# Kernel optimization log

Hardware: AMD Instinct MI355X
Metric: run time of the kernel (lower is better)

Reference implementation:

```python
import jax, jax.numpy as jnp
import numpy as np

N, D, L = 8192, 512, 32


def setup_inputs() -> dict:
    key = jax.random.key(0)
    ks = jax.random.split(key, 14)
    def lin(k, fan_out, fan_in):
        s = 1.0 / np.sqrt(fan_in)
        kw, kb = jax.random.split(k)
        W = jax.random.uniform(kw, (fan_out, fan_in), jnp.float32, -s, s)
        b = jax.random.uniform(kb, (fan_out,), jnp.float32, -s, s)
        return W, b
    xs = jax.random.normal(ks[0], (N, D), jnp.float32)
    W1, b1 = lin(ks[1], 64, D)
    W2, b2 = lin(ks[2], 32, 64)
    W3, b3 = lin(ks[3], L, 32)
    D1, d1 = lin(ks[4], 32, L)
    D2, d2 = lin(ks[5], 64, 32)
    D3, d3 = lin(ks[6], D, 64)
    return {"xs": xs, "W1": W1, "b1": b1, "W2": W2, "b2": b2, "W3": W3, "b3": b3,
            "D1": D1, "d1": d1, "D2": D2, "d2": d2, "D3": D3, "d3": d3}


def reference(xs, W1, b1, W2, b2, W3, b3, D1, d1, D2, d2, D3, d3):
    # Nearest-neighbor (excluding self). Squared distances via Gram trick;
    # argmin over squared dists == argmin over norms, and the original's
    # +1e6*eye diagonal penalty == masking the diagonal with +inf.
    sq = jnp.sum(xs * xs, axis=-1)                     # [N]
    d2m = sq[:, None] + sq[None, :] - 2.0 * (xs @ xs.T)  # [N, N]
    d2m = d2m + jnp.where(jnp.eye(xs.shape[0], dtype=bool), jnp.inf, 0.0)
    closest = jnp.argmin(d2m, axis=1)                  # [N]
    x0s = xs[closest]                                  # [N, D]

    def encoder(x):  # batched tiny MLP, linear in jvp
        h = jax.nn.relu(x @ W1.T + b1)
        h = jax.nn.relu(h @ W2.T + b2)
        return h @ W3.T + b3

    # First-order Taylor expansion around the nearest neighbor:
    # z = f(x0) + Jf(x0) @ (x - x0)
    z0, dz = jax.jvp(encoder, (x0s,), (xs - x0s,))
    zs = z0 + dz                                       # [N, L]

    h = jax.nn.relu(zs @ D1.T + d1)
    h = jax.nn.relu(h @ D2.T + d2)
    x_hats = h @ D3.T + d3                             # [N, D]
    return (x_hats, zs)
```

## Files before the change

### kernel.cpp

```cpp
#include <hip/hip_runtime.h>
#include <hip/hip_bf16.h>

#define NROWS 8192
#define DIM 512
#define NSLOT 194
#define KMASK 0xFFFFE000u
#define QSCALE 21.0f
#define QD2 (-2.0f / (QSCALE * QSCALE))

typedef __attribute__((ext_vector_type(8))) short bf16x8;
typedef __attribute__((ext_vector_type(4))) float f32x4;
typedef __attribute__((ext_vector_type(4))) int i32x4;
typedef __attribute__((ext_vector_type(8))) unsigned short u16x8;

__device__ __forceinline__ float bf2f(unsigned short u) {
    return __uint_as_float(((unsigned int)u) << 16);
}
__device__ __forceinline__ unsigned short f2bf(float f) {
    unsigned int b = __float_as_uint(f);
    return (unsigned short)((b + 0x7FFFu + ((b >> 16) & 1u)) >> 16);
}
__device__ __forceinline__ unsigned char f2i8(float x) {
    float s = x * QSCALE;
    s = fminf(fmaxf(s, -127.f), 127.f);
    const int q = __float2int_rn(s);
    return (unsigned char)(q & 0xFF);
}
__device__ __forceinline__ unsigned int fkey(float f) {
    unsigned int b = __float_as_uint(f);
    return (b & 0x80000000u) ? ~b : (b | 0x80000000u);
}
__device__ __forceinline__ float unfkey(unsigned int u) {
    unsigned int b = (u & 0x80000000u) ? (u ^ 0x80000000u) : ~u;
    return __uint_as_float(b);
}
__device__ __forceinline__ unsigned int minu(unsigned int a, unsigned int b) {
    return a < b ? a : b;
}
__device__ __forceinline__ unsigned int maxu(unsigned int a, unsigned int b) {
    return a > b ? a : b;
}
__device__ __forceinline__ unsigned long long min64(unsigned long long a,
                                                    unsigned long long b) {
    return a < b ? a : b;
}
__device__ __forceinline__ float bcastf(float v, int k) {
    return __uint_as_float((unsigned int)__builtin_amdgcn_readlane(__float_as_uint(v), k));
}

__device__ __forceinline__ void split3(const float* v, u16x8& h8, u16x8& m8, u16x8& l8) {
#pragma unroll
    for (int j = 0; j < 8; ++j) {
        const float x = v[j];
        const unsigned short h = f2bf(x);
        const float r1 = x - bf2f(h);
        const unsigned short m = f2bf(r1);
        const float r2 = r1 - bf2f(m);
        h8[j] = h; m8[j] = m; l8[j] = f2bf(r2);
    }
}
__device__ __forceinline__ void split2(const float* v, u16x8& h8, u16x8& l8) {
#pragma unroll
    for (int j = 0; j < 8; ++j) {
        const float x = v[j];
        const unsigned short h = f2bf(x);
        h8[j] = h; l8[j] = f2bf(x - bf2f(h));
    }
}

__global__ __launch_bounds__(256) void k_prep_p(const float* __restrict__ xs,
                                                unsigned char* __restrict__ x8,
                                                float* __restrict__ sq,
                                                const float* __restrict__ W1,
                                                float* __restrict__ P) {
    __shared__ __align__(16) unsigned short lAh[64 * 32], lAm[64 * 32], lAl[64 * 32];
    __shared__ __align__(16) unsigned short lWh[64 * 32], lWm[64 * 32], lWl[64 * 32];
    const int tid = threadIdx.x;
    if (blockIdx.x >= 128) {
        const int wave = tid >> 6, lane = tid & 63;
        const int row = (blockIdx.x - 128) * 4 + wave;
        const float4* xr = (const float4*)(xs + (size_t)row * DIM);
        const float4 a = xr[2 * lane], b = xr[2 * lane + 1];
        float v[8] = {a.x, a.y, a.z, a.w, b.x, b.y, b.z, b.w};
        unsigned long long pk8 = 0ull;
        float s = 0.f;
#pragma unroll
        for (int i = 0; i < 8; ++i) {
            pk8 |= ((unsigned long long)f2i8(v[i])) << (8 * i);
            s = fmaf(v[i], v[i], s);
        }
        *(unsigned long long*)(x8 + (size_t)row * DIM + lane * 8) = pk8;
#pragma unroll
        for (int d = 32; d; d >>= 1) s += __shfl_xor(s, d);
        if (lane == 0) sq[row] = s;
        return;
    }
    const int wave = tid >> 6, lane = tid & 63, quad = lane >> 4, ln = lane & 15;
    const int i0 = blockIdx.x * 64;
    const int row = tid >> 2, c = tid & 3;
    const int wofs = row * 32 + ((c + (row >> 1)) & 3) * 8;

    f32x4 acc[4];
#pragma unroll
    for (int ns = 0; ns < 4; ++ns) acc[ns] = (f32x4){0.f, 0.f, 0.f, 0.f};

    const int ar = wave * 16 + ln;
    const int aofs = ar * 32 + ((quad + (ar >> 1)) & 3) * 8;
    int bofs[4];
#pragma unroll
    for (int ns = 0; ns < 4; ++ns) {
        const int br = ns * 16 + ln;
        bofs[ns] = br * 32 + ((quad + (br >> 1)) & 3) * 8;
    }

    for (int kt = 0; kt < 16; ++kt) {
        __syncthreads();
        {
            const float* src = xs + (size_t)(i0 + row) * DIM + kt * 32 + c * 8;
            const float4 f0 = *(const float4*)src, f1 = *(const float4*)(src + 4);
            float v[8] = {f0.x, f0.y, f0.z, f0.w, f1.x, f1.y, f1.z, f1.w};
            u16x8 h8, m8, l8;
            split3(v, h8, m8, l8);
            *(u16x8*)(lAh + wofs) = h8;
            *(u16x8*)(lAm + wofs) = m8;
            *(u16x8*)(lAl + wofs) = l8;
        }
        {
            const float* src = W1 + (size_t)row * DIM + kt * 32 + c * 8;
            const float4 f0 = *(const float4*)src, f1 = *(const float4*)(src + 4);
            float v[8] = {f0.x, f0.y, f0.z, f0.w, f1.x, f1.y, f1.z, f1.w};
            u16x8 h8, m8, l8;
            split3(v, h8, m8, l8);
            *(u16x8*)(lWh + wofs) = h8;
            *(u16x8*)(lWm + wofs) = m8;
            *(u16x8*)(lWl + wofs) = l8;
        }
        __syncthreads();
        const bf16x8 ah = *(const bf16x8*)(lAh + aofs);
        const bf16x8 am = *(const bf16x8*)(lAm + aofs);
        const bf16x8 al = *(const bf16x8*)(lAl + aofs);
#pragma unroll
        for (int ns = 0; ns < 4; ++ns) {
            const bf16x8 bh = *(const bf16x8*)(lWh + bofs[ns]);
            const bf16x8 bm = *(const bf16x8*)(lWm + bofs[ns]);
            const bf16x8 bl = *(const bf16x8*)(lWl + bofs[ns]);
            acc[ns] = __builtin_amdgcn_mfma_f32_16x16x32_bf16(ah, bh, acc[ns], 0, 0, 0);
            acc[ns] = __builtin_amdgcn_mfma_f32_16x16x32_bf16(ah, bm, acc[ns], 0, 0, 0);
            acc[ns] = __builtin_amdgcn_mfma_f32_16x16x32_bf16(am, bh, acc[ns], 0, 0, 0);
            acc[ns] = __builtin_amdgcn_mfma_f32_16x16x32_bf16(am, bm, acc[ns], 0, 0, 0);
            acc[ns] = __builtin_amdgcn_mfma_f32_16x16x32_bf16(ah, bl, acc[ns], 0, 0, 0);
            acc[ns] = __builtin_amdgcn_mfma_f32_16x16x32_bf16(al, bh, acc[ns], 0, 0, 0);
        }
    }
#pragma unroll
    for (int ns = 0; ns < 4; ++ns)
#pragma unroll
        for (int v = 0; v < 4; ++v)
            P[(size_t)(i0 + wave * 16 + quad * 4 + v) * 64 + ns * 16 + ln] = acc[ns][v];
}

__global__ __launch_bounds__(512, 4) void k_nn(const unsigned char* __restrict__ x8,
                                               const float* __restrict__ sq,
                                               unsigned int* __restrict__ rowtab) {
    __shared__ __align__(16) unsigned char lsm[32768];
    unsigned char* lA = lsm;
    unsigned char* lB = lsm + 16384;
    const int tid = threadIdx.x;
    const int wave = tid >> 6, lane = tid & 63, quad = lane >> 4, ln = lane & 15;
    const int b = blockIdx.x;
    const int xcd = b & 7, w = b >> 3;
    const int s = w >> 3, bil = w & 7;
    const int bi = xcd * 8 + bil;
    const int bj = (bi + s) & 63;
    const int i0 = bi * 128, j0 = bj * 128;
    const int m_off = (wave >> 1) * 32, n_off = (wave & 1) * 64;

    const int rl = lane >> 2;
    const int sp = ((lane & 3) - ((rl >> 1) & 3)) & 3;
    const unsigned char* gpA = x8 + (size_t)(i0 + wave * 16 + rl) * DIM + sp * 16;
    const unsigned char* gpB = x8 + (size_t)(j0 + wave * 16 + rl) * DIM + sp * 16;
    unsigned char* dstA = lA + wave * 1024;
    unsigned char* dstB = lB + wave * 1024;

    int aoff[2], boff[4];
#pragma unroll
    for (int ms = 0; ms < 2; ++ms) {
        const int r = m_off + ms * 16 + ln;
        aoff[ms] = r * 64 + ((quad + ((r >> 1) & 3)) & 3) * 16;
    }
#pragma unroll
    for (int ns = 0; ns < 4; ++ns) {
        const int r = n_off + ns * 16 + ln;
        boff[ns] = r * 64 + ((quad + ((r >> 1) & 3)) & 3) * 16;
    }

    i32x4 acc[2][4];
#pragma unroll
    for (int a = 0; a < 2; ++a)
#pragma unroll
        for (int c = 0; c < 4; ++c) acc[a][c] = (i32x4){0, 0, 0, 0};

    __builtin_amdgcn_global_load_lds(
        (const __attribute__((address_space(1))) void*)gpA,
        (__attribute__((address_space(3))) void*)dstA, 16, 0, 0);
    __builtin_amdgcn_global_load_lds(
        (const __attribute__((address_space(1))) void*)gpB,
        (__attribute__((address_space(3))) void*)dstB, 16, 0, 0);

#pragma unroll
    for (int kt = 0; kt < 8; ++kt) {
        __syncthreads();
        if (kt < 7) {
            const int nxt = ((kt + 1) & 1) * 8192;
            __builtin_amdgcn_global_load_lds(
                (const __attribute__((address_space(1))) void*)(gpA + (kt + 1) * 64),
                (__attribute__((address_space(3))) void*)(dstA + nxt), 16, 0, 0);
            __builtin_amdgcn_global_load_lds(
                (const __attribute__((address_space(1))) void*)(gpB + (kt + 1) * 64),
                (__attribute__((address_space(3))) void*)(dstB + nxt), 16, 0, 0);
        }
        const int cur = (kt & 1) * 8192;
        i32x4 av[2], bv[4];
#pragma unroll
        for (int ms = 0; ms < 2; ++ms)
            av[ms] = *(const i32x4*)(lA + cur + aoff[ms]);
#pragma unroll
        for (int ns = 0; ns < 4; ++ns)
            bv[ns] = *(const i32x4*)(lB + cur + boff[ns]);
#pragma unroll
        for (int ms = 0; ms < 2; ++ms)
#pragma unroll
            for (int ns = 0; ns < 4; ++ns)
                acc[ms][ns] = __builtin_amdgcn_mfma_i32_16x16x64_i8(
                    av[ms], bv[ns], acc[ms][ns], 0, 0, 0);
    }
    __syncthreads();

    const bool diag = (s == 0);
    float sqj[4];
#pragma unroll
    for (int ns = 0; ns < 4; ++ns) sqj[ns] = sq[j0 + n_off + ns * 16 + ln];
    float sqi[2][4];
#pragma unroll
    for (int ms = 0; ms < 2; ++ms)
#pragma unroll
        for (int v = 0; v < 4; ++v)
            sqi[ms][v] = sq[i0 + m_off + ms * 16 + quad * 4 + v];

    unsigned long long* rowbuf = (unsigned long long*)(void*)lsm + (size_t)wave * 512;

    unsigned int c1[4], c2[4];
#pragma unroll
    for (int ns = 0; ns < 4; ++ns) { c1[ns] = 0xFFFFFFFFu; c2[ns] = 0xFFFFFFFFu; }

#pragma unroll
    for (int ms = 0; ms < 2; ++ms)
#pragma unroll
        for (int v = 0; v < 4; ++v) {
            const int gi = i0 + m_off + ms * 16 + quad * 4 + v;
            const float si = sqi[ms][v];
            unsigned int rp[4];
#pragma unroll
            for (int ns = 0; ns < 4; ++ns) {
                const int gj = j0 + n_off + ns * 16 + ln;
                float d2 = fmaf((float)acc[ms][ns][v], QD2, si + sqj[ns]);
                if (diag && gj == gi) d2 = __builtin_inff();
                const unsigned int ub = (__float_as_uint(d2) | 0x80000000u) & KMASK;
                rp[ns] = ub | (unsigned int)gj;
                const unsigned int cp = ub | (unsigned int)gi;
                c2[ns] = minu(c2[ns], maxu(c1[ns], cp));
                c1[ns] = minu(c1[ns], cp);
            }
            const unsigned int lo1 = minu(rp[0], rp[1]), hi1 = maxu(rp[0], rp[1]);
            const unsigned int lo2 = minu(rp[2], rp[3]), hi2 = maxu(rp[2], rp[3]);
            const unsigned int p1 = minu(lo1, lo2);
            const unsigned int p2 = minu(maxu(lo1, lo2), minu(hi1, hi2));
            const int rloc = ms * 16 + quad * 4 + v;
            rowbuf[rloc * 16 + ln] = (((unsigned long long)p1) << 32) | p2;
        }
    asm volatile("s_waitcnt lgkmcnt(0)" ::: "memory");

    {
        const int rr = lane & 31, hf = lane >> 5;
        unsigned int p1 = 0xFFFFFFFFu, p2 = 0xFFFFFFFFu;
#pragma unroll
        for (int k = 0; k < 8; ++k) {
            const int pos = hf * 8 + (k ^ (rr & 7));
            const unsigned long long pw = rowbuf[rr * 16 + pos];
            const unsigned int a1 = (unsigned int)(pw >> 32), a2 = (unsigned int)pw;
            p2 = minu(minu(p2, a2), maxu(p1, a1));
            p1 = minu(p1, a1);
        }
        const unsigned long long mine = (((unsigned long long)p1) << 32) | p2;
        const unsigned long long oth = __shfl_xor(mine, 32);
        {
            const unsigned int a1 = (unsigned int)(oth >> 32), a2 = (unsigned int)oth;
            p2 = minu(minu(p2, a2), maxu(p1, a1));
            p1 = minu(p1, a1);
        }
        if (lane < 32) {
            const int gi = i0 + m_off + rr;
            const size_t base = ((size_t)gi * NSLOT + (s * 2 + (wave & 1))) * 2;
            rowtab[base] = p1;
            rowtab[base + 1] = p2;
        }
    }

    if (s > 0) {
#pragma unroll
        for (int ns = 0; ns < 4; ++ns) {
            unsigned int q1 = c1[ns], q2 = c2[ns];
#pragma unroll
            for (int d = 16; d <= 32; d <<= 1) {
                const unsigned long long pr = (((unsigned long long)q1) << 32) | q2;
                const unsigned long long o = __shfl_xor(pr, d);
                const unsigned int a1 = (unsigned int)(o >> 32), a2 = (unsigned int)o;
                q2 = minu(minu(q2, a2), maxu(q1, a1));
                q1 = minu(q1, a1);
            }
            if (lane < 16) {
                const int gj = j0 + n_off + ns * 16 + ln;
                const size_t base =
                    ((size_t)gj * NSLOT + (66 + (s - 1) * 4 + (wave >> 1))) * 2;
                rowtab[base] = q1;
                rowtab[base + 1] = q2;
            }
        }
    }
}

__global__ __launch_bounds__(512, 6) void k_refine_mid(
    const unsigned int* __restrict__ rowtab, const float* __restrict__ xs,
    const float* __restrict__ sq, const float* __restrict__ P,
    const float* __restrict__ b1, const float* __restrict__ W2,
    const float* __restrict__ b2, const float* __restrict__ W3,
    const float* __restrict__ b3, const float* __restrict__ D1,
    const float* __restrict__ d1, const float* __restrict__ D2,
    const float* __restrict__ d2, float* __restrict__ out_zs,
    float* __restrict__ G2) {
    __shared__ float W2T[64 * 33], W3T[32 * 33], D1T[32 * 33], D2T[32 * 65];
    __shared__ float b2f[32], b3f[32], d1f[32], d2f[64];
    __shared__ unsigned int clist[4][64];
    __shared__ int ccnt[4];
    __shared__ unsigned int rowbest[4];
    __shared__ unsigned int nnr_s[4];
    __shared__ float pbuf[4][64 * 8];
    const int tid = threadIdx.x;
    const int wave = tid >> 6, lane = tid & 63;
    const int r = wave & 3, half = wave >> 2;
    const int row = blockIdx.x * 4 + r;
    for (int t = tid; t < 2048; t += 512) { int o = t >> 6, k = t & 63; W2T[k * 33 + o] = W2[t]; }
    for (int t = tid; t < 1024; t += 512) { int o = t >> 5, k = t & 31; W3T[k * 33 + o] = W3[t]; }
    for (int t = tid; t < 1024; t += 512) { int o = t >> 5, k = t & 31; D1T[k * 33 + o] = D1[t]; }
    for (int t = tid; t < 2048; t += 512) { int o = t >> 5, k = t & 31; D2T[k * 65 + o] = D2[t]; }
    if (tid < 32) b2f[tid] = b2[tid];
    else if (tid < 64) b3f[tid - 32] = b3[tid - 32];
    else if (tid < 96) d1f[tid - 64] = d1[tid - 64];
    else if (tid < 160) d2f[tid - 96] = d2[tid - 96];
    if (tid < 4) { ccnt[tid] = 0; rowbest[tid] = 0xFFFFFFFFu; }
    __syncthreads();

    unsigned int vals[4];
    int nv = 0;
    unsigned int best = 0xFFFFFFFFu;
    for (int i = half * 64 + lane; i < NSLOT * 2; i += 128) {
        const unsigned int v = rowtab[(size_t)row * NSLOT * 2 + i];
        vals[nv++] = v;
        best = minu(best, v);
    }
#pragma unroll
    for (int d = 1; d < 64; d <<= 1) best = minu(best, __shfl_xor(best, d));
    if (lane == 0) atomicMin(&rowbest[r], best);
    __syncthreads();
    best = rowbest[r];

    const float dmin = unfkey(best & KMASK);
    const unsigned int tkey = fkey(dmin + 5.0f);
    for (int k = 0; k < nv; ++k)
        if ((vals[k] & KMASK) < tkey) {
            const int p = atomicAdd(&ccnt[r], 1);
            if (p < 64) clist[r][p] = vals[k] & 8191u;
        }
    __syncthreads();
    int cnt = ccnt[r];
    cnt = cnt > 64 ? 64 : cnt;

    const float4* xi = (const float4*)(xs + (size_t)row * DIM);
    const float4 x0 = xi[2 * lane], x1 = xi[2 * lane + 1];
    const float sqi = sq[row];
    const int g8 = lane >> 3;
    float4 cy0 = {0.f, 0.f, 0.f, 0.f}, cy1 = {0.f, 0.f, 0.f, 0.f};
    if (half < cnt) {
        const float4* xj = (const float4*)(xs + (size_t)clist[r][half] * DIM);
        cy0 = xj[2 * lane];
        cy1 = xj[2 * lane + 1];
    }
    for (int c = half; c < cnt; c += 2) {
        float4 ny0 = {0.f, 0.f, 0.f, 0.f}, ny1 = {0.f, 0.f, 0.f, 0.f};
        const int cn = c + 2;
        if (cn < cnt) {
            const float4* xj = (const float4*)(xs + (size_t)clist[r][cn] * DIM);
            ny0 = xj[2 * lane];
            ny1 = xj[2 * lane + 1];
        }
        float dot = 0.f;
        dot = fmaf(x0.x, cy0.x, dot); dot = fmaf(x0.y, cy0.y, dot);
        dot = fmaf(x0.z, cy0.z, dot); dot = fmaf(x0.w, cy0.w, dot);
        dot = fmaf(x1.x, cy1.x, dot); dot = fmaf(x1.y, cy1.y, dot);
        dot = fmaf(x1.z, cy1.z, dot); dot = fmaf(x1.w, cy1.w, dot);
        dot += __shfl_xor(dot, 1);
        dot += __shfl_xor(dot, 2);
        dot += __shfl_xor(dot, 4);
        if ((lane & 7) == 0) pbuf[r][c * 8 + g8] = dot;
        cy0 = ny0;
        cy1 = ny1;
    }
    __syncthreads();

    if (half == 0) {
        unsigned long long key = ~0ull;
        if (lane < cnt) {
            const unsigned int j = clist[r][lane];
            float dot = 0.f;
#pragma unroll
            for (int k = 0; k < 8; ++k)
                dot += pbuf[r][lane * 8 + ((k + lane + (lane >> 3)) & 7)];
            const float d2v = sqi + sq[j] - 2.f * dot;
            key = (((unsigned long long)fkey(d2v)) << 32) | j;
        }
#pragma unroll
        for (int d = 1; d < 64; d <<= 1) key = min64(key, __shfl_xor(key, d));
        if (lane == 0) nnr_s[r] = (unsigned int)(key & 0xFFFFFFFFull) & 8191u;
    }
    __syncthreads();
    if (half == 1) return;
    const unsigned int nnr = nnr_s[r];

    const int o32 = lane & 31;
    const float b1v = b1[lane];
    const float pr = P[(size_t)row * 64 + lane];
    const float p0 = P[(size_t)nnr * 64 + lane];
    const float a1 = p0 + b1v;
    const float u1 = pr - p0;
    const float h1 = fmaxf(a1, 0.f);
    const float th1 = (a1 > 0.f) ? u1 : 0.f;
    float a2 = b2f[o32], u2 = 0.f;
#pragma unroll
    for (int k = 0; k < 64; ++k) {
        const float h = bcastf(h1, k);
        const float t = bcastf(th1, k);
        const float w = W2T[k * 33 + o32];
        a2 = fmaf(h, w, a2);
        u2 = fmaf(t, w, u2);
    }
    const float sv = fmaxf(a2, 0.f) + ((a2 > 0.f) ? u2 : 0.f);
    float z = b3f[o32];
#pragma unroll
    for (int k = 0; k < 32; ++k) z = fmaf(bcastf(sv, k), W3T[k * 33 + o32], z);
    if (lane < 32) out_zs[(size_t)row * 32 + lane] = z;
    float g1 = d1f[o32];
#pragma unroll
    for (int k = 0; k < 32; ++k) g1 = fmaf(bcastf(z, k), D1T[k * 33 + o32], g1);
    g1 = fmaxf(g1, 0.f);
    float g2 = d2f[lane];
#pragma unroll
    for (int k = 0; k < 32; ++k) g2 = fmaf(bcastf(g1, k), D2T[k * 65 + lane], g2);
    g2 = fmaxf(g2, 0.f);
    G2[(size_t)row * 64 + lane] = g2;
}

__global__ __launch_bounds__(512) void k_dec(const float* __restrict__ G2,
                                             const float* __restrict__ D3,
                                             const float* __restrict__ d3,
                                             float* __restrict__ xhat) {
    __shared__ __align__(16) unsigned short lGh[128 * 64], lGl[128 * 64];
    __shared__ __align__(16) unsigned short lDh[128 * 64], lDl[128 * 64];
    const int tid = threadIdx.x, wave = tid >> 6, lane = tid & 63, quad = lane >> 4,
              ln = lane & 15;
    const int i0 = blockIdx.x * 128, nbase = blockIdx.y * 128;
    const int m_off = (wave & 1) * 64, n_off = (wave >> 1) * 32;
#pragma unroll
    for (int r = 0; r < 2; ++r) {
        const int g = r * 512 + tid;
        const int row = g >> 3, cIdx = g & 7, half = cIdx >> 2, cc = cIdx & 3;
        const int wofs = row * 64 + half * 32 + ((cc + (row >> 1)) & 3) * 8;
        {
            const float* src = G2 + (size_t)(i0 + row) * 64 + cIdx * 8;
            const float4 f0 = *(const float4*)src, f1 = *(const float4*)(src + 4);
            float v[8] = {f0.x, f0.y, f0.z, f0.w, f1.x, f1.y, f1.z, f1.w};
            u16x8 h8, l8;
            split2(v, h8, l8);
            *(u16x8*)(lGh + wofs) = h8;
            *(u16x8*)(lGl + wofs) = l8;
        }
        {
            const float* src = D3 + (size_t)(nbase + row) * 64 + cIdx * 8;
            const float4 f0 = *(const float4*)src, f1 = *(const float4*)(src + 4);
            float v[8] = {f0.x, f0.y, f0.z, f0.w, f1.x, f1.y, f1.z, f1.w};
            u16x8 h8, l8;
            split2(v, h8, l8);
            *(u16x8*)(lDh + wofs) = h8;
            *(u16x8*)(lDl + wofs) = l8;
        }
    }
    __syncthreads();
    f32x4 acc[4][2];
#pragma unroll
    for (int a = 0; a < 4; ++a)
#pragma unroll
        for (int c = 0; c < 2; ++c) acc[a][c] = (f32x4){0.f, 0.f, 0.f, 0.f};
#pragma unroll
    for (int kk = 0; kk < 2; ++kk) {
        bf16x8 ah[4], al[4], bh[2], bl[2];
#pragma unroll
        for (int ms = 0; ms < 4; ++ms) {
            const int ar = m_off + ms * 16 + ln;
            const int aofs = ar * 64 + kk * 32 + ((quad + (ar >> 1)) & 3) * 8;
            ah[ms] = *(const bf16x8*)(lGh + aofs);
            al[ms] = *(const bf16x8*)(lGl + aofs);
        }
#pragma unroll
        for (int ns = 0; ns < 2; ++ns) {
            const int br = n_off + ns * 16 + ln;
            const int bofs = br * 64 + kk * 32 + ((quad + (br >> 1)) & 3) * 8;
            bh[ns] = *(const bf16x8*)(lDh + bofs);
            bl[ns] = *(const bf16x8*)(lDl + bofs);
        }
#pragma unroll
        for (int ms = 0; ms < 4; ++ms)
#pragma unroll
            for (int ns = 0; ns < 2; ++ns) {
                acc[ms][ns] = __builtin_amdgcn_mfma_f32_16x16x32_bf16(
                    ah[ms], bh[ns], acc[ms][ns], 0, 0, 0);
                acc[ms][ns] = __builtin_amdgcn_mfma_f32_16x16x32_bf16(
                    ah[ms], bl[ns], acc[ms][ns], 0, 0, 0);
                acc[ms][ns] = __builtin_amdgcn_mfma_f32_16x16x32_bf16(
                    al[ms], bh[ns], acc[ms][ns], 0, 0, 0);
            }
    }
    float d3f[2];
#pragma unroll
    for (int ns = 0; ns < 2; ++ns) d3f[ns] = d3[nbase + n_off + ns * 16 + ln];
#pragma unroll
    for (int ms = 0; ms < 4; ++ms)
#pragma unroll
        for (int ns = 0; ns < 2; ++ns)
#pragma unroll
            for (int v = 0; v < 4; ++v) {
                const int m = m_off + ms * 16 + quad * 4 + v;
                const int n = n_off + ns * 16 + ln;
                xhat[(size_t)(i0 + m) * DIM + nbase + n] = acc[ms][ns][v] + d3f[ns];
            }
}

extern "C" void kernel_launch(void* const* d_in, const int* in_sizes, int n_in,
                              void* d_out, int out_size, void* d_ws, size_t ws_size,
                              hipStream_t stream) {
    const float* xs = (const float*)d_in[0];
    const float* W1 = (const float*)d_in[1];
    const float* b1 = (const float*)d_in[2];
    const float* W2 = (const float*)d_in[3];
    const float* b2 = (const float*)d_in[4];
    const float* W3 = (const float*)d_in[5];
    const float* b3 = (const float*)d_in[6];
    const float* D1 = (const float*)d_in[7];
    const float* d1 = (const float*)d_in[8];
    const float* D2 = (const float*)d_in[9];
    const float* d2 = (const float*)d_in[10];
    const float* D3 = (const float*)d_in[11];
    const float* d3 = (const float*)d_in[12];

    char* ws = (char*)d_ws;
    float* sq = (float*)(ws);
    unsigned char* xs_i8 = (unsigned char*)(ws + 131072);
    float* P = (float*)(ws + 8519680);
    float* G2 = (float*)(ws + 10616832);

    float* xhat = (float*)d_out;
    float* zs = (float*)d_out + (size_t)NROWS * DIM;
    unsigned int* rowtab = (unsigned int*)d_out;

    hipLaunchKernelGGL(k_prep_p, dim3(2176), dim3(256), 0, stream, xs, xs_i8, sq, W1, P);
    hipLaunchKernelGGL(k_nn, dim3(2112), dim3(512), 0, stream, xs_i8, sq, rowtab);
    hipLaunchKernelGGL(k_refine_mid, dim3(2048), dim3(512), 0, stream, rowtab, xs, sq,
                       P, b1, W2, b2, W3, b3, D1, d1, D2, d2, zs, G2);
    hipLaunchKernelGGL(k_dec, dim3(64, 4), dim3(512), 0, stream, G2, D3, d3, xhat);
}
```

Baseline: 170.5 us.

## Move x@W1 projection into k_nn blocks and split accumulator chains in MLP

The split-bf16 x@W1 projection (P) moves out of the prep kernel into the first 128 blocks of the nearest-neighbour kernel, so it runs alongside the int8 distance search instead of in front of it. The prep kernel now only quantises rows and computes squared norms. Separately, the per-row MLP dot products in k_refine_mid use two independent accumulators to shorten FMA dependency chains. As a risk, the projection blocks idle half their 512 threads and compete with the NN blocks for CU slots.

```diff
diff --git a/kernel.cpp b/kernel.cpp
--- a/kernel.cpp
+++ b/kernel.cpp
@@ -68,106 +68,116 @@
     }
 }
 
-__global__ __launch_bounds__(256) void k_prep_p(const float* __restrict__ xs,
-                                                unsigned char* __restrict__ x8,
-                                                float* __restrict__ sq,
-                                                const float* __restrict__ W1,
-                                                float* __restrict__ P) {
-    __shared__ __align__(16) unsigned short lAh[64 * 32], lAm[64 * 32], lAl[64 * 32];
-    __shared__ __align__(16) unsigned short lWh[64 * 32], lWm[64 * 32], lWl[64 * 32];
+__global__ __launch_bounds__(256) void k_prep(const float* __restrict__ xs,
+                                              unsigned char* __restrict__ x8,
+                                              float* __restrict__ sq) {
     const int tid = threadIdx.x;
-    if (blockIdx.x >= 128) {
-        const int wave = tid >> 6, lane = tid & 63;
-        const int row = (blockIdx.x - 128) * 4 + wave;
-        const float4* xr = (const float4*)(xs + (size_t)row * DIM);
-        const float4 a = xr[2 * lane], b = xr[2 * lane + 1];
-        float v[8] = {a.x, a.y, a.z, a.w, b.x, b.y, b.z, b.w};
-        unsigned long long pk8 = 0ull;
-        float s = 0.f;
-#pragma unroll
-        for (int i = 0; i < 8; ++i) {
-            pk8 |= ((unsigned long long)f2i8(v[i])) << (8 * i);
-            s = fmaf(v[i], v[i], s);
-        }
-        *(unsigned long long*)(x8 + (size_t)row * DIM + lane * 8) = pk8;
-#pragma unroll
-        for (int d = 32; d; d >>= 1) s += __shfl_xor(s, d);
-        if (lane == 0) sq[row] = s;
-        return;
-    }
-    const int wave = tid >> 6, lane = tid & 63, quad = lane >> 4, ln = lane & 15;
-    const int i0 = blockIdx.x * 64;
-    const int row = tid >> 2, c = tid & 3;
-    const int wofs = row * 32 + ((c + (row >> 1)) & 3) * 8;
-
-    f32x4 acc[4];
-#pragma unroll
-    for (int ns = 0; ns < 4; ++ns) acc[ns] = (f32x4){0.f, 0.f, 0.f, 0.f};
-
-    const int ar = wave * 16 + ln;
-    const int aofs = ar * 32 + ((quad + (ar >> 1)) & 3) * 8;
-    int bofs[4];
-#pragma unroll
-    for (int ns = 0; ns < 4; ++ns) {
-        const int br = ns * 16 + ln;
-        bofs[ns] = br * 32 + ((quad + (br >> 1)) & 3) * 8;
-    }
-
-    for (int kt = 0; kt < 16; ++kt) {
-        __syncthreads();
-        {
-            const float* src = xs + (size_t)(i0 + row) * DIM + kt * 32 + c * 8;
-            const float4 f0 = *(const float4*)src, f1 = *(const float4*)(src + 4);
-            float v[8] = {f0.x, f0.y, f0.z, f0.w, f1.x, f1.y, f1.z, f1.w};
-            u16x8 h8, m8, l8;
-            split3(v, h8, m8, l8);
-            *(u16x8*)(lAh + wofs) = h8;
-            *(u16x8*)(lAm + wofs) = m8;
-            *(u16x8*)(lAl + wofs) = l8;
-        }
-        {
-            const float* src = W1 + (size_t)row * DIM + kt * 32 + c * 8;
-            const float4 f0 = *(const float4*)src, f1 = *(const float4*)(src + 4);
-            float v[8] = {f0.x, f0.y, f0.z, f0.w, f1.x, f1.y, f1.z, f1.w};
-            u16x8 h8, m8, l8;
-            split3(v, h8, m8, l8);
-            *(u16x8*)(lWh + wofs) = h8;
-            *(u16x8*)(lWm + wofs) = m8;
-            *(u16x8*)(lWl + wofs) = l8;
-        }
-        __syncthreads();
-        const bf16x8 ah = *(const bf16x8*)(lAh + aofs);
-        const bf16x8 am = *(const bf16x8*)(lAm + aofs);
-        const bf16x8 al = *(const bf16x8*)(lAl + aofs);
-#pragma unroll
-        for (int ns = 0; ns < 4; ++ns) {
-            const bf16x8 bh = *(const bf16x8*)(lWh + bofs[ns]);
-            const bf16x8 bm = *(const bf16x8*)(lWm + bofs[ns]);
-            const bf16x8 bl = *(const bf16x8*)(lWl + bofs[ns]);
-            acc[ns] = __builtin_amdgcn_mfma_f32_16x16x32_bf16(ah, bh, acc[ns], 0, 0, 0);
-            acc[ns] = __builtin_amdgcn_mfma_f32_16x16x32_bf16(ah, bm, acc[ns], 0, 0, 0);
-            acc[ns] = __builtin_amdgcn_mfma_f32_16x16x32_bf16(am, bh, acc[ns], 0, 0, 0);
-            acc[ns] = __builtin_amdgcn_mfma_f32_16x16x32_bf16(am, bm, acc[ns], 0, 0, 0);
-            acc[ns] = __builtin_amdgcn_mfma_f32_16x16x32_bf16(ah, bl, acc[ns], 0, 0, 0);
-            acc[ns] = __builtin_amdgcn_mfma_f32_16x16x32_bf16(al, bh, acc[ns], 0, 0, 0);
-        }
-    }
-#pragma unroll
-    for (int ns = 0; ns < 4; ++ns)
-#pragma unroll
-        for (int v = 0; v < 4; ++v)
-            P[(size_t)(i0 + wave * 16 + quad * 4 + v) * 64 + ns * 16 + ln] = acc[ns][v];
+    const int wave = tid >> 6, lane = tid & 63;
+    const int row = blockIdx.x * 4 + wave;
+    const float4* xr = (const float4*)(xs + (size_t)row * DIM);
+    const float4 a = xr[2 * lane], b = xr[2 * lane + 1];
+    float v[8] = {a.x, a.y, a.z, a.w, b.x, b.y, b.z, b.w};
+    unsigned long long pk8 = 0ull;
+    float s = 0.f;
+#pragma unroll
+    for (int i = 0; i < 8; ++i) {
+        pk8 |= ((unsigned long long)f2i8(v[i])) << (8 * i);
+        s = fmaf(v[i], v[i], s);
+    }
+    *(unsigned long long*)(x8 + (size_t)row * DIM + lane * 8) = pk8;
+#pragma unroll
+    for (int d = 32; d; d >>= 1) s += __shfl_xor(s, d);
+    if (lane == 0) sq[row] = s;
 }
 
 __global__ __launch_bounds__(512, 4) void k_nn(const unsigned char* __restrict__ x8,
                                                const float* __restrict__ sq,
-                                               unsigned int* __restrict__ rowtab) {
+                                               unsigned int* __restrict__ rowtab,
+                                               const float* __restrict__ xs,
+                                               const float* __restrict__ W1,
+                                               float* __restrict__ P) {
     __shared__ __align__(16) unsigned char lsm[32768];
+    const int tid = threadIdx.x;
+    const int wave = tid >> 6, lane = tid & 63, quad = lane >> 4, ln = lane & 15;
+
+    if (blockIdx.x < 128) {
+        unsigned short* lAh = (unsigned short*)(lsm);
+        unsigned short* lAm = (unsigned short*)(lsm + 4096);
+        unsigned short* lAl = (unsigned short*)(lsm + 8192);
+        unsigned short* lWh = (unsigned short*)(lsm + 12288);
+        unsigned short* lWm = (unsigned short*)(lsm + 16384);
+        unsigned short* lWl = (unsigned short*)(lsm + 20480);
+        const int i0 = blockIdx.x * 64;
+        const int row = tid >> 2, c = tid & 3;
+        const int wofs = row * 32 + ((c + (row >> 1)) & 3) * 8;
+        f32x4 acc[4];
+#pragma unroll
+        for (int ns = 0; ns < 4; ++ns) acc[ns] = (f32x4){0.f, 0.f, 0.f, 0.f};
+        const int ar = wave * 16 + ln;
+        const int aofs = ar * 32 + ((quad + (ar >> 1)) & 3) * 8;
+        int bofs[4];
+#pragma unroll
+        for (int ns = 0; ns < 4; ++ns) {
+            const int br = ns * 16 + ln;
+            bofs[ns] = br * 32 + ((quad + (br >> 1)) & 3) * 8;
+        }
+        for (int kt = 0; kt < 16; ++kt) {
+            __syncthreads();
+            if (tid < 256) {
+                {
+                    const float* src = xs + (size_t)(i0 + row) * DIM + kt * 32 + c * 8;
+                    const float4 f0 = *(const float4*)src, f1 = *(const float4*)(src + 4);
+                    float v[8] = {f0.x, f0.y, f0.z, f0.w, f1.x, f1.y, f1.z, f1.w};
+                    u16x8 h8, m8, l8;
+                    split3(v, h8, m8, l8);
+                    *(u16x8*)(lAh + wofs) = h8;
+                    *(u16x8*)(lAm + wofs) = m8;
+                    *(u16x8*)(lAl + wofs) = l8;
+                }
+                {
+                    const float* src = W1 + (size_t)row * DIM + kt * 32 + c * 8;
+                    const float4 f0 = *(const float4*)src, f1 = *(const float4*)(src + 4);
+                    float v[8] = {f0.x, f0.y, f0.z, f0.w, f1.x, f1.y, f1.z, f1.w};
+                    u16x8 h8, m8, l8;
+                    split3(v, h8, m8, l8);
+                    *(u16x8*)(lWh + wofs) = h8;
+                    *(u16x8*)(lWm + wofs) = m8;
+                    *(u16x8*)(lWl + wofs) = l8;
+                }
+            }
+            __syncthreads();
+            if (tid < 256) {
+                const bf16x8 ah = *(const bf16x8*)(lAh + aofs);
+                const bf16x8 am = *(const bf16x8*)(lAm + aofs);
+                const bf16x8 al = *(const bf16x8*)(lAl + aofs);
+#pragma unroll
+                for (int ns = 0; ns < 4; ++ns) {
+                    const bf16x8 bh = *(const bf16x8*)(lWh + bofs[ns]);
+                    const bf16x8 bm = *(const bf16x8*)(lWm + bofs[ns]);
+                    const bf16x8 bl = *(const bf16x8*)(lWl + bofs[ns]);
+                    acc[ns] = __builtin_amdgcn_mfma_f32_16x16x32_bf16(ah, bh, acc[ns], 0, 0, 0);
+                    acc[ns] = __builtin_amdgcn_mfma_f32_16x16x32_bf16(ah, bm, acc[ns], 0, 0, 0);
+                    acc[ns] = __builtin_amdgcn_mfma_f32_16x16x32_bf16(am, bh, acc[ns], 0, 0, 0);
+                    acc[ns] = __builtin_amdgcn_mfma_f32_16x16x32_bf16(am, bm, acc[ns], 0, 0, 0);
+                    acc[ns] = __builtin_amdgcn_mfma_f32_16x16x32_bf16(ah, bl, acc[ns], 0, 0, 0);
+                    acc[ns] = __builtin_amdgcn_mfma_f32_16x16x32_bf16(al, bh, acc[ns], 0, 0, 0);
+                }
+            }
+        }
+        if (tid < 256) {
+#pragma unroll
+            for (int ns = 0; ns < 4; ++ns)
+#pragma unroll
+                for (int v = 0; v < 4; ++v)
+                    P[(size_t)(i0 + wave * 16 + quad * 4 + v) * 64 + ns * 16 + ln] =
+                        acc[ns][v];
+        }
+        return;
+    }
+
     unsigned char* lA = lsm;
     unsigned char* lB = lsm + 16384;
-    const int tid = threadIdx.x;
-    const int wave = tid >> 6, lane = tid & 63, quad = lane >> 4, ln = lane & 15;
-    const int b = blockIdx.x;
+    const int b = blockIdx.x - 128;
     const int xcd = b & 7, w = b >> 3;
     const int s = w >> 3, bil = w & 7;
     const int bi = xcd * 8 + bil;
@@ -444,28 +454,42 @@
     const float u1 = pr - p0;
     const float h1 = fmaxf(a1, 0.f);
     const float th1 = (a1 > 0.f) ? u1 : 0.f;
-    float a2 = b2f[o32], u2 = 0.f;
-#pragma unroll
-    for (int k = 0; k < 64; ++k) {
-        const float h = bcastf(h1, k);
-        const float t = bcastf(th1, k);
-        const float w = W2T[k * 33 + o32];
-        a2 = fmaf(h, w, a2);
-        u2 = fmaf(t, w, u2);
-    }
+    float a2a = b2f[o32], a2b = 0.f, u2a = 0.f, u2b = 0.f;
+#pragma unroll
+    for (int k = 0; k < 64; k += 2) {
+        const float ha = bcastf(h1, k), hb = bcastf(h1, k + 1);
+        const float ta = bcastf(th1, k), tb = bcastf(th1, k + 1);
+        const float wa = W2T[k * 33 + o32], wb = W2T[(k + 1) * 33 + o32];
+        a2a = fmaf(ha, wa, a2a);
+        a2b = fmaf(hb, wb, a2b);
+        u2a = fmaf(ta, wa, u2a);
+        u2b = fmaf(tb, wb, u2b);
+    }
+    const float a2 = a2a + a2b;
+    const float u2 = u2a + u2b;
     const float sv = fmaxf(a2, 0.f) + ((a2 > 0.f) ? u2 : 0.f);
-    float z = b3f[o32];
-#pragma unroll
-    for (int k = 0; k < 32; ++k) z = fmaf(bcastf(sv, k), W3T[k * 33 + o32], z);
+    float za = b3f[o32], zb = 0.f;
+#pragma unroll
+    for (int k = 0; k < 32; k += 2) {
+        za = fmaf(bcastf(sv, k), W3T[k * 33 + o32], za);
+        zb = fmaf(bcastf(sv, k + 1), W3T[(k + 1) * 33 + o32], zb);
+    }
+    const float z = za + zb;
     if (lane < 32) out_zs[(size_t)row * 32 + lane] = z;
-    float g1 = d1f[o32];
-#pragma unroll
-    for (int k = 0; k < 32; ++k) g1 = fmaf(bcastf(z, k), D1T[k * 33 + o32], g1);
-    g1 = fmaxf(g1, 0.f);
-    float g2 = d2f[lane];
-#pragma unroll
-    for (int k = 0; k < 32; ++k) g2 = fmaf(bcastf(g1, k), D2T[k * 65 + lane], g2);
-    g2 = fmaxf(g2, 0.f);
+    float g1a = d1f[o32], g1b = 0.f;
+#pragma unroll
+    for (int k = 0; k < 32; k += 2) {
+        g1a = fmaf(bcastf(z, k), D1T[k * 33 + o32], g1a);
+        g1b = fmaf(bcastf(z, k + 1), D1T[(k + 1) * 33 + o32], g1b);
+    }
+    const float g1 = fmaxf(g1a + g1b, 0.f);
+    float g2a = d2f[lane], g2b = 0.f;
+#pragma unroll
+    for (int k = 0; k < 32; k += 2) {
+        g2a = fmaf(bcastf(g1, k), D2T[k * 65 + lane], g2a);
+        g2b = fmaf(bcastf(g1, k + 1), D2T[(k + 1) * 65 + lane], g2b);
+    }
+    const float g2 = fmaxf(g2a + g2b, 0.f);
     G2[(size_t)row * 64 + lane] = g2;
 }
 
@@ -580,8 +604,9 @@
     float* zs = (float*)d_out + (size_t)NROWS * DIM;
     unsigned int* rowtab = (unsigned int*)d_out;
 
-    hipLaunchKernelGGL(k_prep_p, dim3(2176), dim3(256), 0, stream, xs, xs_i8, sq, W1, P);
-    hipLaunchKernelGGL(k_nn, dim3(2112), dim3(512), 0, stream, xs_i8, sq, rowtab);
+    hipLaunchKernelGGL(k_prep, dim3(2048), dim3(256), 0, stream, xs, xs_i8, sq);
+    hipLaunchKernelGGL(k_nn, dim3(2240), dim3(512), 0, stream, xs_i8, sq, rowtab, xs,
+                       W1, P);
     hipLaunchKernelGGL(k_refine_mid, dim3(2048), dim3(512), 0, stream, rowtab, xs, sq,
                        P, b1, W2, b2, W3, b3, D1, d1, D2, d2, zs, G2);
     hipLaunchKernelGGL(k_dec, dim3(64, 4), dim3(512), 0, stream, G2, D3, d3, xhat);
```

Result: faster. 156.4 us, median of 2 (-8.2%).
